# Performance work log

Hardware: AMD Instinct MI355X
Metric: run time of the kernel (lower is better)

## Reference

```python
import jax, jax.numpy as jnp
import numpy as np

B, T, D, N, L, SCALE = 16, 4096, 256, 16, 4, 2
EPS_LN = 1e-5


def setup_inputs() -> dict:
    key = jax.random.key(0)
    ks = jax.random.split(key, 20)
    def w(k, shape, s):
        return jax.random.normal(k, shape, jnp.float32) * s
    inp = {"x": jax.random.normal(ks[0], (B, T, D), jnp.float32)}
    for i, pfx in enumerate(("fwd", "bwd")):
        b = 1 + i * 4
        inp[f"{pfx}_norm_w"] = jnp.ones((L, D), jnp.float32)
        inp[f"{pfx}_norm_b"] = jnp.zeros((L, D), jnp.float32)
        inp[f"{pfx}_dw"] = w(ks[b], (L, D, D), 1.0 / np.sqrt(D))
        inp[f"{pfx}_db"] = jnp.zeros((L, D), jnp.float32)
        inp[f"{pfx}_alog"] = w(ks[b + 1], (L, D, N), 0.02)
        inp[f"{pfx}_bparam"] = w(ks[b + 2], (L, D, N), 0.02)
        inp[f"{pfx}_ow"] = w(ks[b + 3], (L, D, D), 1.0 / np.sqrt(D))
        inp[f"{pfx}_ob"] = jnp.zeros((L, D), jnp.float32)
    inp["merge_w"] = w(ks[17], (2 * D, D), 1.0 / np.sqrt(2 * D))
    inp["merge_b"] = jnp.zeros((D,), jnp.float32)
    inp["scale"] = SCALE
    return inp


def _layernorm(x, g, b):
    m = x.mean(-1, keepdims=True)
    v = ((x - m) ** 2).mean(-1, keepdims=True)
    return (x - m) * jax.lax.rsqrt(v + EPS_LN) * g + b


def _ssm(x, dw, db, alog, bparam, ow, ob):
    # x: [B, Ts, D]; selective SSM recurrence over time (sequential scan).
    delta = jax.nn.softplus(x @ dw + db)          # [B, Ts, D]
    a_pos = jax.nn.softplus(alog) + 1e-4          # [D, N]
    s0 = jnp.zeros((x.shape[0], x.shape[2], a_pos.shape[1]), x.dtype)
    def step(state, td):
        x_t, d_t = td                             # each [B, D]
        state = jnp.exp(-d_t[:, :, None] * a_pos) * state + (d_t * x_t)[:, :, None] * bparam
        return state, state.sum(-1)               # y_t: [B, D]
    _, y = jax.lax.scan(step, s0, (jnp.swapaxes(x, 0, 1), jnp.swapaxes(delta, 0, 1)))
    return jnp.swapaxes(y, 0, 1) @ ow + ob


def _stack(x, nw, nb, dw, db, alog, bparam, ow, ob):
    # PreNorm -> SSM -> Residual, n_layers times (dropout=0 / eval)
    for l in range(nw.shape[0]):
        x = x + _ssm(_layernorm(x, nw[l], nb[l]), dw[l], db[l], alog[l], bparam[l], ow[l], ob[l])
    return x


def _upsample_linear(x, target_len):
    # matches F.interpolate(mode='linear', align_corners=False) on [B, Ts, D]
    in_len = x.shape[1]
    if in_len == target_len:
        return x
    pos = (jnp.arange(target_len, dtype=jnp.float32) + 0.5) * (in_len / target_len) - 0.5
    pos = jnp.clip(pos, 0.0, in_len - 1)
    lo = jnp.floor(pos).astype(jnp.int32)
    hi = jnp.minimum(lo + 1, in_len - 1)
    w = (pos - lo)[None, :, None]
    return x[:, lo, :] * (1.0 - w) + x[:, hi, :] * w


def reference(x, fwd_norm_w, fwd_norm_b, fwd_dw, fwd_db, fwd_alog, fwd_bparam, fwd_ow, fwd_ob,
              bwd_norm_w, bwd_norm_b, bwd_dw, bwd_db, bwd_alog, bwd_bparam, bwd_ow, bwd_ob,
              merge_w, merge_b, scale):
    target_len = x.shape[1]
    if scale != 1:
        b_, t_, d_ = x.shape
        # avg_pool1d(kernel=scale, stride=scale); T divisible by scale so ceil_mode is a no-op
        x_s = x.reshape(b_, t_ // scale, scale, d_).mean(2)
    else:
        x_s = x
    fwd = _stack(x_s, fwd_norm_w, fwd_norm_b, fwd_dw, fwd_db, fwd_alog, fwd_bparam, fwd_ow, fwd_ob)
    bwd = jnp.flip(_stack(jnp.flip(x_s, 1), bwd_norm_w, bwd_norm_b, bwd_dw, bwd_db, bwd_alog, bwd_bparam, bwd_ow, bwd_ob), 1)
    merged = jnp.concatenate([fwd, bwd], -1) @ merge_w + merge_b
    return _upsample_linear(merged, target_len)
```

## Files before the change

### kernel.cpp

```cpp
#include <hip/hip_runtime.h>


typedef __attribute__((ext_vector_type(8))) short short8;
typedef __attribute__((ext_vector_type(4))) float f32x4;

#define TS 2048
#define NSEQ_D 8192u
#define NCH 32
#define CLEN 64
#define LDSP 72

#if __has_builtin(__builtin_amdgcn_exp2f)
#define EXP2F(x) __builtin_amdgcn_exp2f(x)
#else
#define EXP2F(x) exp2f(x)
#endif
#if __has_builtin(__builtin_amdgcn_logf)
#define LOG2F(x) __builtin_amdgcn_logf(x)
#else
#define LOG2F(x) log2f(x)
#endif
#define LOG2E 1.44269504088896f
#define LN2 0.69314718055995f

__device__ __forceinline__ unsigned short f2bf(float f) {
  unsigned u = __float_as_uint(f);
  u = u + 0x7FFFu + ((u >> 16) & 1u);
  return (unsigned short)(u >> 16);
}
__device__ __forceinline__ float bf2f(unsigned short h) {
  return __uint_as_float(((unsigned)h) << 16);
}
__device__ __forceinline__ float softplus_fast(float x) {
  float e = EXP2F(-fabsf(x) * LOG2E);
  return fmaxf(x, 0.f) + LN2 * LOG2F(1.f + e);
}

__global__ __launch_bounds__(256) void wconv_kernel(
    const float* __restrict__ fdw, const float* __restrict__ bdw,
    const float* __restrict__ fow, const float* __restrict__ bow,
    const float* __restrict__ mw,
    unsigned short* __restrict__ dwT, unsigned short* __restrict__ owT,
    unsigned short* __restrict__ mT) {
  unsigned idx = blockIdx.x * 256u + threadIdx.x;
  if (idx < 524288u) {
    unsigned dir = idx >> 18, l = (idx >> 16) & 3u, n = (idx >> 8) & 255u, k = idx & 255u;
    const float* s = dir ? bdw : fdw;
    dwT[idx] = f2bf(s[((l << 8) + k) * 256u + n]);
  } else if (idx < 1048576u) {
    unsigned r = idx - 524288u;
    unsigned dir = r >> 18, l = (r >> 16) & 3u, n = (r >> 8) & 255u, k = r & 255u;
    const float* s = dir ? bow : fow;
    owT[r] = f2bf(s[((l << 8) + k) * 256u + n]);
  } else {
    unsigned r = idx - 1048576u;
    unsigned n = r >> 9, k = r & 511u;
    mT[r] = f2bf(mw[(k << 8) + n]);
  }
}

__global__ __launch_bounds__(256) void ln0_kernel(
    const float* __restrict__ x, float* __restrict__ xw,
    unsigned short* __restrict__ xn,
    const float* __restrict__ fnw, const float* __restrict__ fnb,
    const float* __restrict__ bnw, const float* __restrict__ bnb) {
  unsigned row = (blockIdx.x << 2) + (threadIdx.x >> 6);
  unsigned lane = threadIdx.x & 63u;
  unsigned b = row >> 11, jj = row & 2047u;
  const float4* x4 = (const float4*)x;
  float4 v0 = x4[(((b << 12) + (jj << 1)) << 6) + lane];
  float4 v1 = x4[(((b << 12) + (jj << 1) + 1u) << 6) + lane];
  float4 p;
  p.x = 0.5f * (v0.x + v1.x); p.y = 0.5f * (v0.y + v1.y);
  p.z = 0.5f * (v0.z + v1.z); p.w = 0.5f * (v0.w + v1.w);
  float s = p.x + p.y + p.z + p.w;
  float q = p.x * p.x + p.y * p.y + p.z * p.z + p.w * p.w;
  for (int o = 32; o > 0; o >>= 1) { s += __shfl_xor(s, o); q += __shfl_xor(q, o); }
  float m = s * (1.f / 256.f);
  float rstd = rsqrtf(q * (1.f / 256.f) - m * m + 1e-5f);

  unsigned r0 = ((b << 11) + jj) << 6;
  unsigned r1 = ((((16u + b) << 11) + (2047u - jj)) << 6);
  ((float4*)xw)[r0 + lane] = p;
  ((float4*)xw)[r1 + lane] = p;

  unsigned dd = lane << 2;
  float zx = (p.x - m) * rstd, zy = (p.y - m) * rstd, zz = (p.z - m) * rstd, zw = (p.w - m) * rstd;
  ushort4 o0 = make_ushort4(
      f2bf(zx * fnw[dd] + fnb[dd]), f2bf(zy * fnw[dd + 1] + fnb[dd + 1]),
      f2bf(zz * fnw[dd + 2] + fnb[dd + 2]), f2bf(zw * fnw[dd + 3] + fnb[dd + 3]));
  ushort4 o1 = make_ushort4(
      f2bf(zx * bnw[dd] + bnb[dd]), f2bf(zy * bnw[dd + 1] + bnb[dd + 1]),
      f2bf(zz * bnw[dd + 2] + bnb[dd + 2]), f2bf(zw * bnw[dd + 3] + bnb[dd + 3]));
  ((ushort4*)xn)[r0 + lane] = o0;
  ((ushort4*)xn)[r1 + lane] = o1;
}

__global__ __launch_bounds__(256) void ln_kernel(
    const float* __restrict__ xw, unsigned short* __restrict__ xn,
    const float* __restrict__ fnw, const float* __restrict__ fnb,
    const float* __restrict__ bnw, const float* __restrict__ bnb, int l) {
  unsigned row = (blockIdx.x << 2) + (threadIdx.x >> 6);
  unsigned lane = threadIdx.x & 63u;
  unsigned dir = row >> 15;
  const float* g = (dir ? bnw : fnw) + (l << 8);
  const float* bb = (dir ? bnb : fnb) + (l << 8);
  float4 v = ((const float4*)xw)[(row << 6) + lane];
  float s = v.x + v.y + v.z + v.w;
  float q = v.x * v.x + v.y * v.y + v.z * v.z + v.w * v.w;
  for (int o = 32; o > 0; o >>= 1) { s += __shfl_xor(s, o); q += __shfl_xor(q, o); }
  float m = s * (1.f / 256.f);
  float var = q * (1.f / 256.f) - m * m;
  float r = rsqrtf(var + 1e-5f);
  unsigned dd = lane << 2;
  ushort4 o4 = make_ushort4(
      f2bf((v.x - m) * r * g[dd + 0] + bb[dd + 0]),
      f2bf((v.y - m) * r * g[dd + 1] + bb[dd + 1]),
      f2bf((v.z - m) * r * g[dd + 2] + bb[dd + 2]),
      f2bf((v.w - m) * r * g[dd + 3] + bb[dd + 3]));
  ((ushort4*)xn)[(row << 6) + lane] = o4;
}

template <int MODE>
__global__ __launch_bounds__(256) void gemm_layer_k(
    const unsigned short* __restrict__ Abf, const unsigned short* __restrict__ WT,
    const float* __restrict__ bias_f, const float* __restrict__ bias_b, int l,
    unsigned short* __restrict__ delta_out, float* __restrict__ xw) {
  __shared__ __align__(16) unsigned short As[64 * LDSP];
  __shared__ __align__(16) unsigned short Bs[256 * LDSP];
  const int tid = threadIdx.x;
  const int lane = tid & 63, wave = tid >> 6;
  const int wm = wave >> 1, wn = wave & 1;
  const int lrow = lane & 15, lhi = lane >> 4;
  const int r0 = blockIdx.x << 6;
  const int dir = r0 >> 15;
  const unsigned short* W = WT + (((dir << 2) + l) << 16);
  const float* bias = (dir ? bias_b : bias_f) + (l << 8);

  const int arow = tid >> 2, ako = (tid & 3) << 4;
  const int brow = tid;

  f32x4 acc[2][8] = {};

  for (int it = 0; it < 4; ++it) {
    const int k0 = it << 6;
    __syncthreads();
    {
      int4 ra[2], rb[8];
      const unsigned ab = (unsigned)(r0 + arow) * 256u + (unsigned)(k0 + ako);
#pragma unroll
      for (int i = 0; i < 2; ++i) ra[i] = *(const int4*)&Abf[ab + (unsigned)(i << 3)];
      const unsigned bb = (unsigned)brow * 256u + (unsigned)k0;
#pragma unroll
      for (int i = 0; i < 8; ++i) rb[i] = *(const int4*)&W[bb + (unsigned)(i << 3)];
#pragma unroll
      for (int i = 0; i < 2; ++i) *(int4*)&As[arow * LDSP + ako + (i << 3)] = ra[i];
#pragma unroll
      for (int i = 0; i < 8; ++i) *(int4*)&Bs[brow * LDSP + (i << 3)] = rb[i];
    }
    __syncthreads();
#pragma unroll
    for (int kk = 0; kk < 2; ++kk) {
      short8 af[2], bfr[8];
#pragma unroll
      for (int m = 0; m < 2; ++m)
        af[m] = *(const short8*)&As[((wm << 5) + (m << 4) + lrow) * LDSP + (kk << 5) + (lhi << 3)];
#pragma unroll
      for (int n = 0; n < 8; ++n)
        bfr[n] = *(const short8*)&Bs[((wn << 7) + (n << 4) + lrow) * LDSP + (kk << 5) + (lhi << 3)];
#pragma unroll
      for (int m = 0; m < 2; ++m)
#pragma unroll
        for (int n = 0; n < 8; ++n)
          acc[m][n] = __builtin_amdgcn_mfma_f32_16x16x32_bf16(af[m], bfr[n], acc[m][n], 0, 0, 0);
    }
  }

#pragma unroll
  for (int m = 0; m < 2; ++m) {
#pragma unroll
    for (int n = 0; n < 8; ++n) {
      const int col = (wn << 7) + (n << 4) + lrow;
      const float bv = bias[col];
#pragma unroll
      for (int j = 0; j < 4; ++j) {
        const unsigned grow = (unsigned)(r0 + (wm << 5) + (m << 4) + (lhi << 2) + j);
        float v = acc[m][n][j] + bv;
        if (MODE == 0) {
          delta_out[grow * 256u + (unsigned)col] = f2bf(softplus_fast(v));
        } else {
          xw[grow * 256u + (unsigned)col] += v;
        }
      }
    }
  }
}

__global__ __launch_bounds__(256) void scan_pass1(
    const unsigned short* __restrict__ delta, const unsigned short* __restrict__ xn,
    float4* __restrict__ SP,
    const float* __restrict__ alog_f, const float* __restrict__ alog_b, int l) {
  const unsigned gid = blockIdx.x * 256u + threadIdx.x;
  const unsigned seq = gid & (NSEQ_D - 1u);
  const unsigned c = gid >> 13;
  const int d = seq & 255;
  const unsigned seqrow = seq >> 8;
  const int dir = seq >> 12;
  const float* alog = (dir ? alog_b : alog_f) + (((l << 8) + d) << 4);

  float c2[16];
#pragma unroll
  for (int q = 0; q < 4; ++q) {
    float4 av = ((const float4*)alog)[q];
    c2[q * 4 + 0] = -(softplus_fast(av.x) + 1e-4f) * LOG2E;
    c2[q * 4 + 1] = -(softplus_fast(av.y) + 1e-4f) * LOG2E;
    c2[q * 4 + 2] = -(softplus_fast(av.z) + 1e-4f) * LOG2E;
    c2[q * 4 + 3] = -(softplus_fast(av.w) + 1e-4f) * LOG2E;
  }

  const unsigned base = (seqrow << 19) + (((unsigned)c << 6) << 8) + (unsigned)d;
  float s[16];
#pragma unroll
  for (int n = 0; n < 16; ++n) s[n] = 0.f;
  float dsum = 0.f;

  for (int tt = 0; tt < CLEN; tt += 8) {
    const unsigned bb = base + ((unsigned)tt << 8);
    unsigned short dv[8], xv[8];
#pragma unroll
    for (int k = 0; k < 8; ++k) dv[k] = delta[bb + ((unsigned)k << 8)];
#pragma unroll
    for (int k = 0; k < 8; ++k) xv[k] = xn[bb + ((unsigned)k << 8)];
#pragma unroll
    for (int k = 0; k < 8; ++k) {
      float dt = bf2f(dv[k]);
      float u = dt * bf2f(xv[k]);
      dsum += dt;
#pragma unroll
      for (int n = 0; n < 16; ++n)
        s[n] = fmaf(EXP2F(c2[n] * dt), s[n], u);
    }
  }

  float4* o = &SP[(size_t)gid << 3];
#pragma unroll
  for (int q = 0; q < 4; ++q) {
    float4 v; v.x = s[q * 4]; v.y = s[q * 4 + 1]; v.z = s[q * 4 + 2]; v.w = s[q * 4 + 3];
    o[q] = v;
  }
#pragma unroll
  for (int q = 0; q < 4; ++q) {
    float4 v;
    v.x = EXP2F(c2[q * 4 + 0] * dsum); v.y = EXP2F(c2[q * 4 + 1] * dsum);
    v.z = EXP2F(c2[q * 4 + 2] * dsum); v.w = EXP2F(c2[q * 4 + 3] * dsum);
    o[4 + q] = v;
  }
}

__global__ __launch_bounds__(256) void scan_mid(float* __restrict__ SP) {
  const unsigned t = blockIdx.x * 256u + threadIdx.x;
  const unsigned seq = t >> 4;
  const unsigned n = t & 15u;
  float* base = SP + (size_t)seq * 32 + n;
  const size_t cstride = (size_t)NSEQ_D * 32;
  float sg = 0.f;
  for (int c = 0; c < NCH - 1; ++c) {
    float S = base[c * cstride];
    float P = base[c * cstride + 16];
    base[c * cstride] = sg;
    sg = fmaf(P, sg, S);
  }
  base[(NCH - 1) * cstride] = sg;
}

__global__ __launch_bounds__(256) void scan_pass2(
    const unsigned short* __restrict__ delta, const unsigned short* __restrict__ xn,
    unsigned short* __restrict__ y, const float4* __restrict__ SP,
    const float* __restrict__ alog_f, const float* __restrict__ alog_b,
    const float* __restrict__ bp_f, const float* __restrict__ bp_b, int l) {
  const unsigned gid = blockIdx.x * 256u + threadIdx.x;
  const unsigned seq = gid & (NSEQ_D - 1u);
  const unsigned c = gid >> 13;
  const int d = seq & 255;
  const unsigned seqrow = seq >> 8;
  const int dir = seq >> 12;
  const float* alog = (dir ? alog_b : alog_f) + (((l << 8) + d) << 4);
  const float* bpp = (dir ? bp_b : bp_f) + (((l << 8) + d) << 4);

  float c2[16], bp[16];
#pragma unroll
  for (int q = 0; q < 4; ++q) {
    float4 av = ((const float4*)alog)[q];
    c2[q * 4 + 0] = -(softplus_fast(av.x) + 1e-4f) * LOG2E;
    c2[q * 4 + 1] = -(softplus_fast(av.y) + 1e-4f) * LOG2E;
    c2[q * 4 + 2] = -(softplus_fast(av.z) + 1e-4f) * LOG2E;
    c2[q * 4 + 3] = -(softplus_fast(av.w) + 1e-4f) * LOG2E;
    float4 bv = ((const float4*)bpp)[q];
    bp[q * 4 + 0] = bv.x; bp[q * 4 + 1] = bv.y; bp[q * 4 + 2] = bv.z; bp[q * 4 + 3] = bv.w;
  }

  float s[16];
  {
    const float4* sg = &SP[(size_t)gid << 3];
    float4 v0 = sg[0], v1 = sg[1], v2 = sg[2], v3 = sg[3];
    s[0] = v0.x; s[1] = v0.y; s[2] = v0.z; s[3] = v0.w;
    s[4] = v1.x; s[5] = v1.y; s[6] = v1.z; s[7] = v1.w;
    s[8] = v2.x; s[9] = v2.y; s[10] = v2.z; s[11] = v2.w;
    s[12] = v3.x; s[13] = v3.y; s[14] = v3.z; s[15] = v3.w;
  }

  const unsigned base = (seqrow << 19) + (((unsigned)c << 6) << 8) + (unsigned)d;

  for (int tt = 0; tt < CLEN; tt += 8) {
    const unsigned bb = base + ((unsigned)tt << 8);
    unsigned short dv[8], xv[8];
#pragma unroll
    for (int k = 0; k < 8; ++k) dv[k] = delta[bb + ((unsigned)k << 8)];
#pragma unroll
    for (int k = 0; k < 8; ++k) xv[k] = xn[bb + ((unsigned)k << 8)];
#pragma unroll
    for (int k = 0; k < 8; ++k) {
      float dt = bf2f(dv[k]);
      float u = dt * bf2f(xv[k]);
#pragma unroll
      for (int n = 0; n < 16; ++n)
        s[n] = fmaf(EXP2F(c2[n] * dt), s[n], u);
      float ya = bp[0] * s[0], yb = bp[1] * s[1], yc = bp[2] * s[2], yd = bp[3] * s[3];
      ya = fmaf(bp[4], s[4], ya);   yb = fmaf(bp[5], s[5], yb);
      yc = fmaf(bp[6], s[6], yc);   yd = fmaf(bp[7], s[7], yd);
      ya = fmaf(bp[8], s[8], ya);   yb = fmaf(bp[9], s[9], yb);
      yc = fmaf(bp[10], s[10], yc); yd = fmaf(bp[11], s[11], yd);
      ya = fmaf(bp[12], s[12], ya); yb = fmaf(bp[13], s[13], yb);
      yc = fmaf(bp[14], s[14], yc); yd = fmaf(bp[15], s[15], yd);
      float ys = (ya + yb) + (yc + yd);
      y[bb + ((unsigned)k << 8)] = f2bf(ys);
    }
  }
}

__global__ __launch_bounds__(256) void gemm_merge_k(
    const float* __restrict__ xw, const unsigned short* __restrict__ MT,
    const float* __restrict__ mb, float* __restrict__ merged) {
  __shared__ __align__(16) unsigned short As[64 * LDSP];
  __shared__ __align__(16) unsigned short Bs[256 * LDSP];
  const int tid = threadIdx.x;
  const int lane = tid & 63, wave = tid >> 6;
  const int wm = wave >> 1, wn = wave & 1;
  const int lrow = lane & 15, lhi = lane >> 4;
  const int r0 = blockIdx.x << 6;

  const int arow = tid >> 2, afo = (tid & 3) << 4;
  const int brow = tid;

  f32x4 acc[2][8] = {};

  for (int it = 0; it < 8; ++it) {
    const int k0 = it << 6;
    __syncthreads();
    {
      int gr = r0 + arow;
      int b = gr >> 11, t = gr & 2047;
      unsigned srcrow = (k0 < 256) ? (unsigned)(b * 2048 + t)
                                   : (unsigned)((16 + b) * 2048 + (2047 - t));
      const float4* ap = (const float4*)&xw[srcrow * 256u + (unsigned)((k0 & 255) + afo)];
      float4 rf[4];
#pragma unroll
      for (int i = 0; i < 4; ++i) rf[i] = ap[i];
      int4 rb[8];
      const unsigned bb = (unsigned)brow * 512u + (unsigned)k0;
#pragma unroll
      for (int i = 0; i < 8; ++i) rb[i] = *(const int4*)&MT[bb + (unsigned)(i << 3)];
#pragma unroll
      for (int i = 0; i < 2; ++i) {
        float4 f0 = rf[2 * i], f1 = rf[2 * i + 1];
        short8 pk;
        pk[0] = (short)f2bf(f0.x); pk[1] = (short)f2bf(f0.y);
        pk[2] = (short)f2bf(f0.z); pk[3] = (short)f2bf(f0.w);
        pk[4] = (short)f2bf(f1.x); pk[5] = (short)f2bf(f1.y);
        pk[6] = (short)f2bf(f1.z); pk[7] = (short)f2bf(f1.w);
        *(short8*)&As[arow * LDSP + afo + (i << 3)] = pk;
      }
#pragma unroll
      for (int i = 0; i < 8; ++i) *(int4*)&Bs[brow * LDSP + (i << 3)] = rb[i];
    }
    __syncthreads();
#pragma unroll
    for (int kk = 0; kk < 2; ++kk) {
      short8 af[2], bfr[8];
#pragma unroll
      for (int m = 0; m < 2; ++m)
        af[m] = *(const short8*)&As[((wm << 5) + (m << 4) + lrow) * LDSP + (kk << 5) + (lhi << 3)];
#pragma unroll
      for (int n = 0; n < 8; ++n)
        bfr[n] = *(const short8*)&Bs[((wn << 7) + (n << 4) + lrow) * LDSP + (kk << 5) + (lhi << 3)];
#pragma unroll
      for (int m = 0; m < 2; ++m)
#pragma unroll
        for (int n = 0; n < 8; ++n)
          acc[m][n] = __builtin_amdgcn_mfma_f32_16x16x32_bf16(af[m], bfr[n], acc[m][n], 0, 0, 0);
    }
  }

#pragma unroll
  for (int m = 0; m < 2; ++m) {
#pragma unroll
    for (int n = 0; n < 8; ++n) {
      const int col = (wn << 7) + (n << 4) + lrow;
      const float bv = mb[col];
#pragma unroll
      for (int j = 0; j < 4; ++j) {
        const unsigned grow = (unsigned)(r0 + (wm << 5) + (m << 4) + (lhi << 2) + j);
        merged[grow * 256u + (unsigned)col] = acc[m][n][j] + bv;
      }
    }
  }
}

__global__ __launch_bounds__(256) void up_kernel(const float4* __restrict__ m4,
                                                 float4* __restrict__ out4) {
  unsigned idx = blockIdx.x * 256u + threadIdx.x;
  unsigned d4 = idx & 63u;
  unsigned t = (idx >> 6) & 4095u;
  unsigned b = idx >> 18;
  unsigned j = t >> 1;
  unsigned lo, hi; float wlo, whi;
  if (t & 1u) { lo = j; hi = (j < 2047u) ? j + 1u : 2047u; wlo = 0.75f; whi = 0.25f; }
  else { lo = j ? j - 1u : 0u; hi = j; wlo = 0.25f; whi = 0.75f; }
  float4 a = m4[((b << 11) + lo) * 64u + d4];
  float4 c = m4[((b << 11) + hi) * 64u + d4];
  float4 o;
  o.x = wlo * a.x + whi * c.x; o.y = wlo * a.y + whi * c.y;
  o.z = wlo * a.z + whi * c.z; o.w = wlo * a.w + whi * c.w;
  out4[((b << 12) + t) * 64u + d4] = o;
}

extern "C" void kernel_launch(void* const* d_in, const int* in_sizes, int n_in,
                              void* d_out, int out_size, void* d_ws, size_t ws_size,
                              hipStream_t stream) {
  const float* x    = (const float*)d_in[0];
  const float* fnw  = (const float*)d_in[1];
  const float* fnb  = (const float*)d_in[2];
  const float* fdw  = (const float*)d_in[3];
  const float* fdb  = (const float*)d_in[4];
  const float* falog = (const float*)d_in[5];
  const float* fbp  = (const float*)d_in[6];
  const float* fow  = (const float*)d_in[7];
  const float* fob  = (const float*)d_in[8];
  const float* bnw  = (const float*)d_in[9];
  const float* bnb  = (const float*)d_in[10];
  const float* bdw  = (const float*)d_in[11];
  const float* bdb  = (const float*)d_in[12];
  const float* balog = (const float*)d_in[13];
  const float* bbp  = (const float*)d_in[14];
  const float* bow  = (const float*)d_in[15];
  const float* bob  = (const float*)d_in[16];
  const float* mw   = (const float*)d_in[17];
  const float* mb   = (const float*)d_in[18];

  char* ws = (char*)d_ws;
  const size_t SZ = 33554432;
  unsigned short* xn_bf  = (unsigned short*)(ws);
  unsigned short* delta  = (unsigned short*)(ws + SZ);
  unsigned short* y_bf   = (unsigned short*)(ws + 2 * SZ);
  float4* SP             = (float4*)(ws + 3 * SZ);
  unsigned short* dwT    = (unsigned short*)(ws + 4 * SZ);
  unsigned short* owT    = dwT + 524288;
  unsigned short* mergeT = owT + 524288;
  float* merged          = (float*)delta;
  float* xw              = (float*)d_out;

  wconv_kernel<<<4608, 256, 0, stream>>>(fdw, bdw, fow, bow, mw, dwT, owT, mergeT);
  ln0_kernel<<<8192, 256, 0, stream>>>(x, xw, xn_bf, fnw, fnb, bnw, bnb);

  for (int l = 0; l < 4; ++l) {
    if (l > 0)
      ln_kernel<<<16384, 256, 0, stream>>>(xw, xn_bf, fnw, fnb, bnw, bnb, l);
    gemm_layer_k<0><<<1024, 256, 0, stream>>>(xn_bf, dwT, fdb, bdb, l, delta, nullptr);
    scan_pass1<<<32 * (NCH - 1), 256, 0, stream>>>(delta, xn_bf, SP, falog, balog, l);
    scan_mid<<<512, 256, 0, stream>>>((float*)SP);
    scan_pass2<<<32 * NCH, 256, 0, stream>>>(delta, xn_bf, y_bf, SP, falog, balog, fbp, bbp, l);
    gemm_layer_k<1><<<1024, 256, 0, stream>>>(y_bf, owT, fob, bob, l, nullptr, xw);
  }

  gemm_merge_k<<<512, 256, 0, stream>>>(xw, mergeT, mb, merged);
  up_kernel<<<16384, 256, 0, stream>>>((const float4*)merged, (float4*)d_out);
}
```

Baseline: 776.2 us.

## Split SSM scan state dims across lane pairs with DPP reduction

Each scan sequence is now handled by two adjacent threads, each owning 8 of the 16 state dimensions, doubling the thread count for scan_pass1 and scan_pass2. The output sum over states is completed with a DPP lane swap and written by one lane. This halves per-thread registers and the serial work per thread to improve latency hiding, at the cost of duplicated delta/x loads and an extra cross-lane op per timestep.

```diff
diff --git a/kernel.cpp b/kernel.cpp
--- a/kernel.cpp
+++ b/kernel.cpp
@@ -196,21 +196,23 @@
   }
 }
 
+
 __global__ __launch_bounds__(256) void scan_pass1(
     const unsigned short* __restrict__ delta, const unsigned short* __restrict__ xn,
     float4* __restrict__ SP,
     const float* __restrict__ alog_f, const float* __restrict__ alog_b, int l) {
   const unsigned gid = blockIdx.x * 256u + threadIdx.x;
-  const unsigned seq = gid & (NSEQ_D - 1u);
-  const unsigned c = gid >> 13;
+  const unsigned h = gid & 1u;
+  const unsigned seq = (gid >> 1) & (NSEQ_D - 1u);
+  const unsigned c = gid >> 14;
   const int d = seq & 255;
   const unsigned seqrow = seq >> 8;
   const int dir = seq >> 12;
-  const float* alog = (dir ? alog_b : alog_f) + (((l << 8) + d) << 4);
-
-  float c2[16];
-#pragma unroll
-  for (int q = 0; q < 4; ++q) {
+  const float* alog = (dir ? alog_b : alog_f) + (((l << 8) + d) << 4) + (h << 3);
+
+  float c2[8];
+#pragma unroll
+  for (int q = 0; q < 2; ++q) {
     float4 av = ((const float4*)alog)[q];
     c2[q * 4 + 0] = -(softplus_fast(av.x) + 1e-4f) * LOG2E;
     c2[q * 4 + 1] = -(softplus_fast(av.y) + 1e-4f) * LOG2E;
@@ -219,9 +221,9 @@
   }
 
   const unsigned base = (seqrow << 19) + (((unsigned)c << 6) << 8) + (unsigned)d;
-  float s[16];
-#pragma unroll
-  for (int n = 0; n < 16; ++n) s[n] = 0.f;
+  float s[8];
+#pragma unroll
+  for (int n = 0; n < 8; ++n) s[n] = 0.f;
   float dsum = 0.f;
 
   for (int tt = 0; tt < CLEN; tt += 8) {
@@ -237,24 +239,22 @@
       float u = dt * bf2f(xv[k]);
       dsum += dt;
 #pragma unroll
-      for (int n = 0; n < 16; ++n)
+      for (int n = 0; n < 8; ++n)
         s[n] = fmaf(EXP2F(c2[n] * dt), s[n], u);
     }
   }
 
-  float4* o = &SP[(size_t)gid << 3];
-#pragma unroll
-  for (int q = 0; q < 4; ++q) {
-    float4 v; v.x = s[q * 4]; v.y = s[q * 4 + 1]; v.z = s[q * 4 + 2]; v.w = s[q * 4 + 3];
-    o[q] = v;
-  }
-#pragma unroll
-  for (int q = 0; q < 4; ++q) {
-    float4 v;
-    v.x = EXP2F(c2[q * 4 + 0] * dsum); v.y = EXP2F(c2[q * 4 + 1] * dsum);
-    v.z = EXP2F(c2[q * 4 + 2] * dsum); v.w = EXP2F(c2[q * 4 + 3] * dsum);
-    o[4 + q] = v;
-  }
+  float4* o = &SP[(((size_t)c * NSEQ_D + seq) << 3) + (h << 1)];
+  float4 v0, v1;
+  v0.x = s[0]; v0.y = s[1]; v0.z = s[2]; v0.w = s[3];
+  v1.x = s[4]; v1.y = s[5]; v1.z = s[6]; v1.w = s[7];
+  o[0] = v0; o[1] = v1;
+  float4 p0, p1;
+  p0.x = EXP2F(c2[0] * dsum); p0.y = EXP2F(c2[1] * dsum);
+  p0.z = EXP2F(c2[2] * dsum); p0.w = EXP2F(c2[3] * dsum);
+  p1.x = EXP2F(c2[4] * dsum); p1.y = EXP2F(c2[5] * dsum);
+  p1.z = EXP2F(c2[6] * dsum); p1.w = EXP2F(c2[7] * dsum);
+  o[4] = p0; o[5] = p1;
 }
 
 __global__ __launch_bounds__(256) void scan_mid(float* __restrict__ SP) {
@@ -279,34 +279,34 @@
     const float* __restrict__ alog_f, const float* __restrict__ alog_b,
     const float* __restrict__ bp_f, const float* __restrict__ bp_b, int l) {
   const unsigned gid = blockIdx.x * 256u + threadIdx.x;
-  const unsigned seq = gid & (NSEQ_D - 1u);
-  const unsigned c = gid >> 13;
+  const unsigned h = gid & 1u;
+  const unsigned seq = (gid >> 1) & (NSEQ_D - 1u);
+  const unsigned c = gid >> 14;
   const int d = seq & 255;
   const unsigned seqrow = seq >> 8;
   const int dir = seq >> 12;
-  const float* alog = (dir ? alog_b : alog_f) + (((l << 8) + d) << 4);
-  const float* bpp = (dir ? bp_b : bp_f) + (((l << 8) + d) << 4);
-
-  float c2[16], bp[16];
-#pragma unroll
-  for (int q = 0; q < 4; ++q) {
+  const float* alog = (dir ? alog_b : alog_f) + (((l << 8) + d) << 4) + (h << 3);
+  const float* bpp = (dir ? bp_b : bp_f) + (((l << 8) + d) << 4) + (h << 3);
+
+  float c2[8], bp[8];
+#pragma unroll
+  for (int q = 0; q < 2; ++q) {
     float4 av = ((const float4*)alog)[q];
     c2[q * 4 + 0] = -(softplus_fast(av.x) + 1e-4f) * LOG2E;
     c2[q * 4 + 1] = -(softplus_fast(av.y) + 1e-4f) * LOG2E;
     c2[q * 4 + 2] = -(softplus_fast(av.z) + 1e-4f) * LOG2E;
     c2[q * 4 + 3] = -(softplus_fast(av.w) + 1e-4f) * LOG2E;
     float4 bv = ((const float4*)bpp)[q];
-    bp[q * 4 + 0] = bv.x; bp[q * 4 + 1] = bv.y; bp[q * 4 + 2] = bv.z; bp[q * 4 + 3] = bv.w;
-  }
-
-  float s[16];
+    bp[q * 4 + 0] = bv.x; bp[q * 4 + 1] = bv.y;
+    bp[q * 4 + 2] = bv.z; bp[q * 4 + 3] = bv.w;
+  }
+
+  float s[8];
   {
-    const float4* sg = &SP[(size_t)gid << 3];
-    float4 v0 = sg[0], v1 = sg[1], v2 = sg[2], v3 = sg[3];
+    const float4* sg = &SP[(((size_t)c * NSEQ_D + seq) << 3) + (h << 1)];
+    float4 v0 = sg[0], v1 = sg[1];
     s[0] = v0.x; s[1] = v0.y; s[2] = v0.z; s[3] = v0.w;
     s[4] = v1.x; s[5] = v1.y; s[6] = v1.z; s[7] = v1.w;
-    s[8] = v2.x; s[9] = v2.y; s[10] = v2.z; s[11] = v2.w;
-    s[12] = v3.x; s[13] = v3.y; s[14] = v3.z; s[15] = v3.w;
   }
 
   const unsigned base = (seqrow << 19) + (((unsigned)c << 6) << 8) + (unsigned)d;
@@ -323,17 +323,16 @@
       float dt = bf2f(dv[k]);
       float u = dt * bf2f(xv[k]);
 #pragma unroll
-      for (int n = 0; n < 16; ++n)
+      for (int n = 0; n < 8; ++n)
         s[n] = fmaf(EXP2F(c2[n] * dt), s[n], u);
-      float ya = bp[0] * s[0], yb = bp[1] * s[1], yc = bp[2] * s[2], yd = bp[3] * s[3];
-      ya = fmaf(bp[4], s[4], ya);   yb = fmaf(bp[5], s[5], yb);
-      yc = fmaf(bp[6], s[6], yc);   yd = fmaf(bp[7], s[7], yd);
-      ya = fmaf(bp[8], s[8], ya);   yb = fmaf(bp[9], s[9], yb);
-      yc = fmaf(bp[10], s[10], yc); yd = fmaf(bp[11], s[11], yd);
-      ya = fmaf(bp[12], s[12], ya); yb = fmaf(bp[13], s[13], yb);
-      yc = fmaf(bp[14], s[14], yc); yd = fmaf(bp[15], s[15], yd);
-      float ys = (ya + yb) + (yc + yd);
-      y[bb + ((unsigned)k << 8)] = f2bf(ys);
+      float ya = bp[0] * s[0], yb = bp[1] * s[1];
+      ya = fmaf(bp[2], s[2], ya); yb = fmaf(bp[3], s[3], yb);
+      ya = fmaf(bp[4], s[4], ya); yb = fmaf(bp[5], s[5], yb);
+      ya = fmaf(bp[6], s[6], ya); yb = fmaf(bp[7], s[7], yb);
+      float ys = ya + yb;
+      int pr = __builtin_amdgcn_update_dpp(0, __float_as_int(ys), 0xB1, 0xf, 0xf, 1);
+      ys += __int_as_float(pr);
+      if (h == 0) y[bb + ((unsigned)k << 8)] = f2bf(ys);
     }
   }
 }
@@ -476,9 +475,9 @@
     if (l > 0)
       ln_kernel<<<16384, 256, 0, stream>>>(xw, xn_bf, fnw, fnb, bnw, bnb, l);
     gemm_layer_k<0><<<1024, 256, 0, stream>>>(xn_bf, dwT, fdb, bdb, l, delta, nullptr);
-    scan_pass1<<<32 * (NCH - 1), 256, 0, stream>>>(delta, xn_bf, SP, falog, balog, l);
+    scan_pass1<<<64 * (NCH - 1), 256, 0, stream>>>(delta, xn_bf, SP, falog, balog, l);
     scan_mid<<<512, 256, 0, stream>>>((float*)SP);
-    scan_pass2<<<32 * NCH, 256, 0, stream>>>(delta, xn_bf, y_bf, SP, falog, balog, fbp, bbp, l);
+    scan_pass2<<<64 * NCH, 256, 0, stream>>>(delta, xn_bf, y_bf, SP, falog, balog, fbp, bbp, l);
     gemm_layer_k<1><<<1024, 256, 0, stream>>>(y_bf, owT, fob, bob, l, nullptr, xw);
   }
 
```

Measured after the change: 808.5 us. 1.04x slower.

## Double-buffer GEMM tiles with direct global-to-LDS loads and XOR swizzle

Applied to the files above, without the earlier changes.

Replaces the register-staged global-to-LDS copy in the layer GEMM with async global_load_lds direct copies into two LDS buffers, prefetching the next K tile while computing the current one. The padded LDS layout is replaced by an XOR swizzle to avoid bank conflicts. The aim is to hide global load latency and free registers. LDS usage doubles (~80KB), which may reduce occupancy, and correctness relies on the barrier ordering with async LDS writes.

```diff
diff --git a/kernel.cpp b/kernel.cpp
--- a/kernel.cpp
+++ b/kernel.cpp
@@ -34,6 +34,12 @@
 __device__ __forceinline__ float softplus_fast(float x) {
   float e = EXP2F(-fabsf(x) * LOG2E);
   return fmaxf(x, 0.f) + LN2 * LOG2F(1.f + e);
+}
+
+__device__ __forceinline__ void gld16(const unsigned short* g, unsigned short* l) {
+  __builtin_amdgcn_global_load_lds(
+      (const __attribute__((address_space(1))) void*)g,
+      (__attribute__((address_space(3))) void*)l, 16, 0, 0);
 }
 
 __global__ __launch_bounds__(256) void wconv_kernel(
@@ -126,8 +132,8 @@
     const unsigned short* __restrict__ Abf, const unsigned short* __restrict__ WT,
     const float* __restrict__ bias_f, const float* __restrict__ bias_b, int l,
     unsigned short* __restrict__ delta_out, float* __restrict__ xw) {
-  __shared__ __align__(16) unsigned short As[64 * LDSP];
-  __shared__ __align__(16) unsigned short Bs[256 * LDSP];
+  __shared__ __align__(16) unsigned short As[2][64 * 64];
+  __shared__ __align__(16) unsigned short Bs[2][256 * 64];
   const int tid = threadIdx.x;
   const int lane = tid & 63, wave = tid >> 6;
   const int wm = wave >> 1, wn = wave & 1;
@@ -137,43 +143,53 @@
   const unsigned short* W = WT + (((dir << 2) + l) << 16);
   const float* bias = (dir ? bias_b : bias_f) + (l << 8);
 
-  const int arow = tid >> 2, ako = (tid & 3) << 4;
-  const int brow = tid;
-
   f32x4 acc[2][8] = {};
 
-  for (int it = 0; it < 4; ++it) {
-    const int k0 = it << 6;
-    __syncthreads();
-    {
-      int4 ra[2], rb[8];
-      const unsigned ab = (unsigned)(r0 + arow) * 256u + (unsigned)(k0 + ako);
-#pragma unroll
-      for (int i = 0; i < 2; ++i) ra[i] = *(const int4*)&Abf[ab + (unsigned)(i << 3)];
-      const unsigned bb = (unsigned)brow * 256u + (unsigned)k0;
-#pragma unroll
-      for (int i = 0; i < 8; ++i) rb[i] = *(const int4*)&W[bb + (unsigned)(i << 3)];
-#pragma unroll
-      for (int i = 0; i < 2; ++i) *(int4*)&As[arow * LDSP + ako + (i << 3)] = ra[i];
-#pragma unroll
-      for (int i = 0; i < 8; ++i) *(int4*)&Bs[brow * LDSP + (i << 3)] = rb[i];
-    }
-    __syncthreads();
+  auto issue = [&](int p, int k0) {
+#pragma unroll
+    for (int i = 0; i < 2; ++i) {
+      int idx = (i << 8) + tid;
+      int row = idx >> 3, scc = (idx & 7) ^ (row & 7);
+      gld16(&Abf[(unsigned)(r0 + row) * 256u + (unsigned)(k0 + (scc << 3))],
+            &As[p][idx << 3]);
+    }
+#pragma unroll
+    for (int i = 0; i < 8; ++i) {
+      int idx = (i << 8) + tid;
+      int row = idx >> 3, scc = (idx & 7) ^ (row & 7);
+      gld16(&W[(unsigned)row * 256u + (unsigned)(k0 + (scc << 3))],
+            &Bs[p][idx << 3]);
+    }
+  };
+  auto compute = [&](int p) {
 #pragma unroll
     for (int kk = 0; kk < 2; ++kk) {
       short8 af[2], bfr[8];
 #pragma unroll
-      for (int m = 0; m < 2; ++m)
-        af[m] = *(const short8*)&As[((wm << 5) + (m << 4) + lrow) * LDSP + (kk << 5) + (lhi << 3)];
-#pragma unroll
-      for (int n = 0; n < 8; ++n)
-        bfr[n] = *(const short8*)&Bs[((wn << 7) + (n << 4) + lrow) * LDSP + (kk << 5) + (lhi << 3)];
+      for (int m = 0; m < 2; ++m) {
+        int row = (wm << 5) + (m << 4) + lrow;
+        int slot = (row << 3) + (((kk << 2) + lhi) ^ (row & 7));
+        af[m] = *(const short8*)&As[p][slot << 3];
+      }
+#pragma unroll
+      for (int n = 0; n < 8; ++n) {
+        int row = (wn << 7) + (n << 4) + lrow;
+        int slot = (row << 3) + (((kk << 2) + lhi) ^ (row & 7));
+        bfr[n] = *(const short8*)&Bs[p][slot << 3];
+      }
 #pragma unroll
       for (int m = 0; m < 2; ++m)
 #pragma unroll
         for (int n = 0; n < 8; ++n)
           acc[m][n] = __builtin_amdgcn_mfma_f32_16x16x32_bf16(af[m], bfr[n], acc[m][n], 0, 0, 0);
     }
+  };
+
+  issue(0, 0);
+  for (int it = 0; it < 4; ++it) {
+    __syncthreads();
+    if (it < 3) issue((it + 1) & 1, (it + 1) << 6);
+    compute(it & 1);
   }
 
 #pragma unroll
```

Result: faster. 738.0 us (-4.9%).
